# Kernel optimization log

Measured on AMD Instinct MI355X. Metric: run time of the kernel, lower is better.

The kernel has to match this reference:

```python
import jax, jax.numpy as jnp
import numpy as np

H, D = 16, 64  # n_heads, head_dim


def l2norm(t):
    # F.normalize(t, p=2, dim=-1)
    return t / jnp.maximum(jnp.linalg.norm(t, axis=-1, keepdims=True), 1e-12)


def setup_inputs() -> dict:
    key = jax.random.key(0)
    ks = jax.random.split(key, 6)
    B, N, C = 2, 2048, 1024
    x = jax.random.normal(ks[0], (B, N, C), jnp.float32)
    pos_bias = jax.random.normal(ks[1], (1, H, N, N), jnp.float32)
    mask = jnp.zeros((B, 1, 1, N), bool)  # attn_mask: True = masked
    Wqkv = jax.random.normal(ks[2], (C, 3 * H * D), jnp.float32) / np.sqrt(C)
    Wout = jax.random.normal(ks[3], (H * D, C), jnp.float32) / np.sqrt(H * D)
    Wpre = jax.random.normal(ks[4], (H, H), jnp.float32) / np.sqrt(H)   # 1x1 conv pre
    bpre = jnp.zeros((H,), jnp.float32)
    Wpost = jax.random.normal(ks[5], (H, H), jnp.float32) / np.sqrt(H)  # 1x1 conv post
    bpost = jnp.zeros((H,), jnp.float32)
    temperature = jnp.float32(15.5)
    return {"x": x, "pos_bias": pos_bias, "mask": mask, "Wqkv": Wqkv,
            "Wout": Wout, "Wpre": Wpre, "bpre": bpre, "Wpost": Wpost,
            "bpost": bpost, "temperature": temperature}


def reference(x, pos_bias, mask, Wqkv, Wout, Wpre, bpre, Wpost, bpost, temperature):
    B, N, C = x.shape
    # qkv: 'b n (h d qkv) -> qkv b h n d'
    qkv = (x @ Wqkv).reshape(B, N, H, D, 3)
    q = jnp.transpose(qkv[..., 0], (0, 2, 1, 3))  # [B,H,N,D]
    k = jnp.transpose(qkv[..., 1], (0, 2, 1, 3))
    v = jnp.transpose(qkv[..., 2], (0, 2, 1, 3))
    q, k = l2norm(q), l2norm(k)  # cosine_sim
    kv = jnp.stack([k, v], axis=0)  # attach_cache with cache=None
    # temperature-scaled cosine-sim scores
    dots = jnp.einsum('bhid,bhjd->bhij', q, k) * temperature
    # talking heads pre (1x1 conv over head channel)
    dots = jnp.einsum('gh,bhij->bgij', Wpre, dots) + bpre[None, :, None, None]
    dots = dots + pos_bias
    dots = jnp.where(mask, -jnp.finfo(dots.dtype).max, dots)
    attn = jax.nn.softmax(dots, axis=-1)
    # talking heads post
    attn = jnp.einsum('gh,bhij->bgij', Wpost, attn) + bpost[None, :, None, None]
    out = jnp.einsum('bhij,bhjd->bhid', attn, v)  # [B,H,N,D]
    out = jnp.transpose(out, (0, 2, 1, 3)).reshape(B, N, H * D) @ Wout
    return (out, kv)
```

## Files before the change

### kernel.cpp

```cpp
#include <hip/hip_runtime.h>
#include <stdint.h>

typedef __attribute__((ext_vector_type(8))) short bf16x8;
typedef __attribute__((ext_vector_type(4))) float f32x4;
typedef __attribute__((ext_vector_type(4))) short short4v;

#define DEV __device__ __forceinline__
#define L2E 1.4426950408889634f

DEV float bf2f(unsigned short s){ union{unsigned int u; float f;} x; x.u = ((unsigned int)s)<<16; return x.f; }
DEV unsigned short f2bf(float f){ union{float f; unsigned int u;} x; x.f = f; x.u += 0x7fffu + ((x.u>>16)&1u); return (unsigned short)(x.u>>16); }

DEV f32x4 mfma16(bf16x8 a, bf16x8 b, f32x4 c){
  return __builtin_amdgcn_mfma_f32_16x16x32_bf16(a, b, c, 0, 0, 0);
}
DEV f32x4 zero4(){ f32x4 z; z[0]=0.f; z[1]=0.f; z[2]=0.f; z[3]=0.f; return z; }
DEV bf16x8 zerob(){ bf16x8 z; z[0]=0;z[1]=0;z[2]=0;z[3]=0;z[4]=0;z[5]=0;z[6]=0;z[7]=0; return z; }
DEV float fexp2(float x){ float r; asm volatile("v_exp_f32 %0, %1" : "=v"(r) : "v"(x)); return r; }
DEV void barw(){ asm volatile("s_waitcnt lgkmcnt(0)" ::: "memory"); __builtin_amdgcn_s_barrier(); }

__global__ __launch_bounds__(256) void k_f32_to_bf16(const float* __restrict__ in, unsigned short* __restrict__ out, int n4){
  int i = blockIdx.x*256 + threadIdx.x;
  if (i < n4){
    float4 v = ((const float4*)in)[i];
    short4v o; o.x=(short)f2bf(v.x); o.y=(short)f2bf(v.y); o.z=(short)f2bf(v.z); o.w=(short)f2bf(v.w);
    ((short4v*)out)[i] = o;
  }
}

__global__ __launch_bounds__(256) void k_convT(const float* __restrict__ in, unsigned short* __restrict__ out, int R, int Cc){
  __shared__ float t[32][33];
  int c0 = blockIdx.x*32, r0 = blockIdx.y*32;
  int tid = threadIdx.x;
  int row = tid>>3, col4 = (tid&7)*4;
  float4 v = *(const float4*)&in[(size_t)(r0+row)*Cc + c0 + col4];
  t[row][col4+0]=v.x; t[row][col4+1]=v.y; t[row][col4+2]=v.z; t[row][col4+3]=v.w;
  __syncthreads();
  short4v o;
  o.x=(short)f2bf(t[col4+0][row]); o.y=(short)f2bf(t[col4+1][row]);
  o.z=(short)f2bf(t[col4+2][row]); o.w=(short)f2bf(t[col4+3][row]);
  *(short4v*)&out[(size_t)(c0+row)*R + r0 + col4] = o;
}

__global__ __launch_bounds__(256) void k_prep(const float* __restrict__ wpre, const float* __restrict__ wpost,
                                              const float* __restrict__ temp,
                                              unsigned short* __restrict__ wpre_t2,
                                              unsigned short* __restrict__ wpost_b){
  int t = threadIdx.x;
  float T = temp[0];
  wpre_t2[t] = f2bf(wpre[t]*T*L2E);
  wpost_b[t] = f2bf(wpost[t]);
}

__global__ __launch_bounds__(256) void k_maskf(const unsigned char* __restrict__ mask, float* __restrict__ maskf){
  int i = blockIdx.x*256 + threadIdx.x;
  if (i < 4096) maskf[i] = mask[i] ? -1e30f : 0.f;
}

template<int OUTF>
__global__ __launch_bounds__(256,2) void k_gemm(const unsigned short* __restrict__ A, const unsigned short* __restrict__ Bt,
                                                void* __restrict__ Cv, int M, int Nn, int K){
  __shared__ unsigned short As[128][72];
  __shared__ unsigned short Bs[128][72];
  int tid = threadIdx.x;
  int n0 = blockIdx.x*128, m0 = blockIdx.y*128;
  int w = tid>>6, lane = tid&63, lg = lane>>4, lp = lane&15;
  int wm = (w>>1)*64, wn = (w&1)*64;
  f32x4 acc[4][4];
  #pragma unroll
  for (int i=0;i<4;++i)
    #pragma unroll
    for (int j=0;j<4;++j) acc[i][j] = zero4();

  for (int kt=0; kt<K; kt+=64){
    #pragma unroll
    for (int cch=0; cch<4; ++cch){
      int e = tid + cch*256; int r = e>>3, cl = (e&7)*8;
      *(bf16x8*)&As[r][cl] = *(const bf16x8*)&A[(size_t)(m0+r)*K + kt + cl];
      *(bf16x8*)&Bs[r][cl] = *(const bf16x8*)&Bt[(size_t)(n0+r)*K + kt + cl];
    }
    __syncthreads();
    #pragma unroll
    for (int ks=0; ks<2; ++ks){
      bf16x8 a[4], b[4];
      #pragma unroll
      for (int mi=0; mi<4; ++mi) a[mi] = *(const bf16x8*)&As[wm+mi*16+lp][ks*32 + lg*8];
      #pragma unroll
      for (int ni=0; ni<4; ++ni) b[ni] = *(const bf16x8*)&Bs[wn+ni*16+lp][ks*32 + lg*8];
      #pragma unroll
      for (int mi=0; mi<4; ++mi)
        #pragma unroll
        for (int ni=0; ni<4; ++ni)
          acc[mi][ni] = mfma16(a[mi], b[ni], acc[mi][ni]);
    }
    __syncthreads();
  }
  #pragma unroll
  for (int mi=0; mi<4; ++mi)
    #pragma unroll
    for (int ni=0; ni<4; ++ni)
      #pragma unroll
      for (int r=0; r<4; ++r){
        int row = m0+wm+mi*16+lg*4+r, col = n0+wn+ni*16+lp;
        if (OUTF) ((float*)Cv)[(size_t)row*Nn+col] = acc[mi][ni][r];
        else ((unsigned short*)Cv)[(size_t)row*Nn+col] = f2bf(acc[mi][ni][r]);
      }
}

__global__ __launch_bounds__(256) void k_split_norm(const unsigned short* __restrict__ qkv,
                                                    unsigned short* __restrict__ q, unsigned short* __restrict__ k,
                                                    unsigned short* __restrict__ v, float* __restrict__ kv_out){
  int w = threadIdx.x>>6, lane = threadIdx.x&63;
  int widx = blockIdx.x*4 + w;
  int h = widx & 15; int bn = widx >> 4;
  int b = bn >> 11; int n = bn & 2047;
  size_t base = (size_t)bn*3072 + h*192 + lane*3;
  float qv = bf2f(qkv[base]), kvv = bf2f(qkv[base+1]), vv = bf2f(qkv[base+2]);
  float nq = qv*qv, nk = kvv*kvv;
  #pragma unroll
  for (int m=1; m<64; m<<=1){ nq += __shfl_xor(nq, m); nk += __shfl_xor(nk, m); }
  float qn = qv / fmaxf(sqrtf(nq), 1e-12f);
  float kn = kvv / fmaxf(sqrtf(nk), 1e-12f);
  size_t idx = ((size_t)(b*16+h)*2048 + n)*64 + lane;
  q[idx] = f2bf(qn); k[idx] = f2bf(kn); v[idx] = f2bf(vv);
  kv_out[idx] = kn;
  kv_out[4194304 + idx] = vv;
}

__global__ __launch_bounds__(256) void k_transpose_v(const unsigned short* __restrict__ v, unsigned short* __restrict__ vt){
  __shared__ unsigned short t[64][72];
  int bh = blockIdx.y; int n0 = blockIdx.x*64;
  int tid = threadIdx.x;
  #pragma unroll
  for (int cch=0; cch<2; ++cch){
    int e = tid + cch*256; int r = e>>3, c8 = (e&7)*8;
    *(bf16x8*)&t[r][c8] = *(const bf16x8*)&v[((size_t)bh*2048 + n0 + r)*64 + c8];
  }
  __syncthreads();
  #pragma unroll
  for (int cch=0; cch<2; ++cch){
    int e = tid + cch*256; int d = e>>3, nn8 = (e&7)*8;
    bf16x8 o;
    #pragma unroll
    for (int i=0;i<8;++i) o[i] = (short)t[nn8+i][d];
    *(bf16x8*)&vt[((size_t)bh*64 + d)*2048 + n0 + nn8] = o;
  }
}

__global__ __launch_bounds__(256) void k_vsum(const unsigned short* __restrict__ v, float* __restrict__ vsum){
  int bg = blockIdx.x;
  int d = threadIdx.x & 63, part = threadIdx.x>>6;
  float s = 0.f;
  for (int n = part*512; n < part*512+512; ++n) s += bf2f(v[((size_t)bg*2048 + n)*64 + d]);
  __shared__ float red[4][64];
  red[part][d] = s; __syncthreads();
  if (part==0) vsum[bg*64 + d] = red[0][d]+red[1][d]+red[2][d]+red[3][d];
}

__global__ __launch_bounds__(512,2) void k_score3(
    const unsigned short* __restrict__ q,
    const unsigned short* __restrict__ kk,
    const float* __restrict__ pos_bias,
    const float* __restrict__ maskf,
    const unsigned short* __restrict__ wpre_t2,
    const float* __restrict__ bpre,
    unsigned short* __restrict__ Pb,
    float* __restrict__ part_l)
{
  __shared__ __align__(16) char smem[40960];
  const int tid = threadIdx.x;
  const int w = tid>>6, lane = tid&63, lg = lane>>4, lp = lane&15;
  const int bid = blockIdx.x;
  const int qd = bid>>4, r2 = bid&15;
  const int b = r2>>3, n = qd*8 + (r2&7);
  const int it = n>>2, js = n&3;
  const int i0 = it*16, jsb = js*512;
  const int mbase = b*2048;

  bf16x8 qf[2][2];
  #pragma unroll
  for (int hh=0; hh<2; ++hh){
    const unsigned short* qb = q + ((size_t)(b*16+2*w+hh)*2048 + i0 + lp)*64;
    qf[hh][0] = *(const bf16x8*)(qb + lg*8);
    qf[hh][1] = *(const bf16x8*)(qb + 32 + lg*8);
  }
  bf16x8 preA = zerob();
  if (lg < 2) preA = *(const bf16x8*)&wpre_t2[lp*16 + lg*8];
  float bpre_s[4];
  #pragma unroll
  for (int r=0;r<4;++r) bpre_s[r] = bpre[lg*4+r]*L2E - 32.0f;

  float sacc[2][4];
  #pragma unroll
  for (int ii=0;ii<2;++ii)
    #pragma unroll
    for (int r=0;r<4;++r) sacc[ii][r] = 0.f;

  const size_t kbase0 = (size_t)(b*16 + 2*w)*131072;
  const size_t kbase1 = (size_t)(b*16 + 2*w+1)*131072;
  const size_t pb_lane = (size_t)(i0 + 2*w)*2048 + lp;

  bf16x8 k0v[4], k1v[4];
  #pragma unroll
  for (int kf=0; kf<2; ++kf)
    #pragma unroll
    for (int jf=0; jf<2; ++jf){
      size_t off = (size_t)(jsb + jf*16 + lp)*64 + kf*32 + lg*8;
      k0v[kf*2+jf] = *(const bf16x8*)(kk + kbase0 + off);
      k1v[kf*2+jf] = *(const bf16x8*)(kk + kbase1 + off);
    }
  float pbA[4][4], pbB[4][4];
  float mkA0, mkA1, mkB0, mkB1;
  #pragma unroll
  for (int cc=0; cc<4; ++cc)
    #pragma unroll
    for (int r=0;r<4;++r)
      pbA[cc][r] = pos_bias[(size_t)(lg*4+r)*4194304 + pb_lane + (size_t)(cc>>1)*2048 + (cc&1)*16 + jsb];
  mkA0 = maskf[mbase + jsb + lp];
  mkA1 = maskf[mbase + jsb + 16 + lp];

  for (int tt=0; tt<8; ++tt){
    {
      const int j0 = jsb + (2*tt)*32;
      const int j1 = jsb + (2*tt+1)*32;
      char* sbuf = smem;
      f32x4 s0[2], s1[2];
      #pragma unroll
      for (int jf=0;jf<2;++jf){ s0[jf]=zero4(); s1[jf]=zero4(); }
      #pragma unroll
      for (int kf=0; kf<2; ++kf)
        #pragma unroll
        for (int jf=0; jf<2; ++jf){
          s0[jf] = mfma16(qf[0][kf], k0v[kf*2+jf], s0[jf]);
          s1[jf] = mfma16(qf[1][kf], k1v[kf*2+jf], s1[jf]);
        }
      #pragma unroll
      for (int jf=0;jf<2;++jf)
        #pragma unroll
        for (int r=0;r<4;++r){
          int ij = (lg*4+r)*32 + jf*16 + lp;
          unsigned int pk = (unsigned int)f2bf(s0[jf][r]) | ((unsigned int)f2bf(s1[jf][r])<<16);
          *(unsigned int*)(sbuf + ij*40 + w*4) = pk;
        }
      #pragma unroll
      for (int kf=0; kf<2; ++kf)
        #pragma unroll
        for (int jf=0; jf<2; ++jf){
          size_t off = (size_t)(j1 + jf*16 + lp)*64 + kf*32 + lg*8;
          k0v[kf*2+jf] = *(const bf16x8*)(kk + kbase0 + off);
          k1v[kf*2+jf] = *(const bf16x8*)(kk + kbase1 + off);
        }
      #pragma unroll
      for (int cc=0; cc<4; ++cc)
        #pragma unroll
        for (int r=0;r<4;++r)
          pbB[cc][r] = pos_bias[(size_t)(lg*4+r)*4194304 + pb_lane + (size_t)(cc>>1)*2048 + (cc&1)*16 + j1];
      mkB0 = maskf[mbase + j1 + lp];
      mkB1 = maskf[mbase + j1 + 16 + lp];
      barw();
      #pragma unroll
      for (int cc=0; cc<4; ++cc){
        int c = w*4+cc;
        int il = 2*w + (cc>>1);
        int jl = (cc&1)*16 + lp;
        bf16x8 sfrag = zerob();
        if (lg < 2) sfrag = *(const bf16x8*)(sbuf + (c*16+lp)*40 + lg*16);
        f32x4 pa = mfma16(preA, sfrag, zero4());
        float mkj = (cc&1) ? mkA1 : mkA0;
        float pv0 = fexp2(fmaf(pbA[cc][0], L2E, pa[0] + bpre_s[0] + mkj));
        float pv1 = fexp2(fmaf(pbA[cc][1], L2E, pa[1] + bpre_s[1] + mkj));
        float pv2 = fexp2(fmaf(pbA[cc][2], L2E, pa[2] + bpre_s[2] + mkj));
        float pv3 = fexp2(fmaf(pbA[cc][3], L2E, pa[3] + bpre_s[3] + mkj));
        sacc[cc>>1][0] += pv0; sacc[cc>>1][1] += pv1;
        sacc[cc>>1][2] += pv2; sacc[cc>>1][3] += pv3;
        short4v p4;
        p4.x = (short)f2bf(pv0); p4.y = (short)f2bf(pv1);
        p4.z = (short)f2bf(pv2); p4.w = (short)f2bf(pv3);
        *(short4v*)&Pb[(((size_t)(b*2048 + i0+il)*2048) + j0 + jl)*16 + lg*4] = p4;
      }
    }
    {
      const int j0 = jsb + (2*tt+1)*32;
      const int j1 = jsb + ((2*tt+2)&15)*32;
      char* sbuf = smem + 20480;
      f32x4 s0[2], s1[2];
      #pragma unroll
      for (int jf=0;jf<2;++jf){ s0[jf]=zero4(); s1[jf]=zero4(); }
      #pragma unroll
      for (int kf=0; kf<2; ++kf)
        #pragma unroll
        for (int jf=0; jf<2; ++jf){
          s0[jf] = mfma16(qf[0][kf], k0v[kf*2+jf], s0[jf]);
          s1[jf] = mfma16(qf[1][kf], k1v[kf*2+jf], s1[jf]);
        }
      #pragma unroll
      for (int jf=0;jf<2;++jf)
        #pragma unroll
        for (int r=0;r<4;++r){
          int ij = (lg*4+r)*32 + jf*16 + lp;
          unsigned int pk = (unsigned int)f2bf(s0[jf][r]) | ((unsigned int)f2bf(s1[jf][r])<<16);
          *(unsigned int*)(sbuf + ij*40 + w*4) = pk;
        }
      #pragma unroll
      for (int kf=0; kf<2; ++kf)
        #pragma unroll
        for (int jf=0; jf<2; ++jf){
          size_t off = (size_t)(j1 + jf*16 + lp)*64 + kf*32 + lg*8;
          k0v[kf*2+jf] = *(const bf16x8*)(kk + kbase0 + off);
          k1v[kf*2+jf] = *(const bf16x8*)(kk + kbase1 + off);
        }
      #pragma unroll
      for (int cc=0; cc<4; ++cc)
        #pragma unroll
        for (int r=0;r<4;++r)
          pbA[cc][r] = pos_bias[(size_t)(lg*4+r)*4194304 + pb_lane + (size_t)(cc>>1)*2048 + (cc&1)*16 + j1];
      mkA0 = maskf[mbase + j1 + lp];
      mkA1 = maskf[mbase + j1 + 16 + lp];
      barw();
      #pragma unroll
      for (int cc=0; cc<4; ++cc){
        int c = w*4+cc;
        int il = 2*w + (cc>>1);
        int jl = (cc&1)*16 + lp;
        bf16x8 sfrag = zerob();
        if (lg < 2) sfrag = *(const bf16x8*)(sbuf + (c*16+lp)*40 + lg*16);
        f32x4 pa = mfma16(preA, sfrag, zero4());
        float mkj = (cc&1) ? mkB1 : mkB0;
        float pv0 = fexp2(fmaf(pbB[cc][0], L2E, pa[0] + bpre_s[0] + mkj));
        float pv1 = fexp2(fmaf(pbB[cc][1], L2E, pa[1] + bpre_s[1] + mkj));
        float pv2 = fexp2(fmaf(pbB[cc][2], L2E, pa[2] + bpre_s[2] + mkj));
        float pv3 = fexp2(fmaf(pbB[cc][3], L2E, pa[3] + bpre_s[3] + mkj));
        sacc[cc>>1][0] += pv0; sacc[cc>>1][1] += pv1;
        sacc[cc>>1][2] += pv2; sacc[cc>>1][3] += pv3;
        short4v p4;
        p4.x = (short)f2bf(pv0); p4.y = (short)f2bf(pv1);
        p4.z = (short)f2bf(pv2); p4.w = (short)f2bf(pv3);
        *(short4v*)&Pb[(((size_t)(b*2048 + i0+il)*2048) + j0 + jl)*16 + lg*4] = p4;
      }
    }
  }

  #pragma unroll
  for (int ii=0;ii<2;++ii)
    #pragma unroll
    for (int r=0;r<4;++r){
      float v = sacc[ii][r];
      #pragma unroll
      for (int m=1; m<16; m<<=1) v += __shfl_xor(v, m);
      sacc[ii][r] = v;
    }
  if (lp == 0){
    int base = ((b*128+it)*4 + js)*256;
    #pragma unroll
    for (int ii=0;ii<2;++ii){
      float4 st; st.x = sacc[ii][0]; st.y = sacc[ii][1]; st.z = sacc[ii][2]; st.w = sacc[ii][3];
      *(float4*)&part_l[base + (2*w+ii)*16 + lg*4] = st;
    }
  }
}

__global__ __launch_bounds__(512,2) void k_mix3(
    const unsigned short* __restrict__ Pb,
    const unsigned short* __restrict__ vt,
    const unsigned short* __restrict__ wpost_b,
    const float* __restrict__ bpost,
    const float* __restrict__ vsum,
    const float* __restrict__ part_l,
    float* __restrict__ pout0,
    float* __restrict__ pout1)
{
  __shared__ __align__(16) char smem[33792];
  float* linv = (float*)(smem + 32768);
  const int tid = threadIdx.x;
  const int w = tid>>6, lane = tid&63, lg = lane>>4, lp = lane&15;
  const int bid = blockIdx.x;
  const int qd = bid>>4, r2 = bid&15;
  const int b = r2>>3, n = qd*8 + (r2&7);
  const int it = n>>1, js = n&1;
  const int i0 = it*16, jsb = js*1024;

  if (tid < 256){
    int base = ((b*128+it)*4)*256 + tid;
    float sum = part_l[base] + part_l[base+256] + part_l[base+512] + part_l[base+768];
    linv[tid] = 1.f/sum;
  }
  __syncthreads();

  bf16x8 postB[2];
  #pragma unroll
  for (int ii=0;ii<2;++ii){
    postB[ii] = zerob();
    if (lg < 2){
      bf16x8 wf = *(const bf16x8*)&wpost_b[lp*16 + lg*8];
      int i = 2*w+ii;
      #pragma unroll
      for (int e=0;e<8;++e){
        float vsc = bf2f((unsigned short)wf[e]) * linv[i*16 + lg*8 + e];
        postB[ii][e] = (short)f2bf(vsc);
      }
    }
  }

  f32x4 oacc[2][4];
  #pragma unroll
  for (int hh=0; hh<2; ++hh)
    #pragma unroll
    for (int df=0; df<4; ++df) oacc[hh][df] = zero4();

  bf16x8 pA[4], pB[4];
  #pragma unroll
  for (int cc=0; cc<4; ++cc){
    int il = 2*w + (cc>>1);
    pA[cc] = zerob();
    if (lg < 2)
      pA[cc] = *(const bf16x8*)&Pb[(((size_t)(b*2048 + i0+il)*2048) + jsb + (cc&1)*16 + lp)*16 + lg*8];
  }
  __syncthreads();

  for (int tt=0; tt<16; ++tt){
    {
      const int j0 = jsb + (2*tt)*32;
      const int j1 = jsb + (2*tt+1)*32;
      char* abuf = smem;
      #pragma unroll
      for (int cc=0; cc<4; ++cc){
        int il = 2*w + (cc>>1);
        pB[cc] = zerob();
        if (lg < 2)
          pB[cc] = *(const bf16x8*)&Pb[(((size_t)(b*2048 + i0+il)*2048) + j1 + (cc&1)*16 + lp)*16 + lg*8];
      }
      bf16x8 vfr[2][4];
      #pragma unroll
      for (int hh=0; hh<2; ++hh)
        #pragma unroll
        for (int df=0; df<4; ++df)
          vfr[hh][df] = *(const bf16x8*)(vt + ((size_t)(b*16+2*w+hh)*64 + df*16 + lp)*2048 + j0 + lg*8);
      #pragma unroll
      for (int cc=0; cc<4; ++cc){
        int il = 2*w + (cc>>1);
        f32x4 aa = mfma16(pA[cc], postB[cc>>1], zero4());
        short4v av;
        av.x = (short)f2bf(aa[0]); av.y = (short)f2bf(aa[1]);
        av.z = (short)f2bf(aa[2]); av.w = (short)f2bf(aa[3]);
        int row = lp*16 + il;
        int chunk = ((cc&1)*4 + lg) ^ ((lp ^ il)&6);
        *(short4v*)(abuf + row*64 + chunk*8) = av;
      }
      barw();
      #pragma unroll
      for (int hh=0; hh<2; ++hh){
        int gg = 2*w+hh;
        bf16x8 af = *(const bf16x8*)(abuf + (gg*16+lp)*64 + (((lg*2) ^ ((gg^lp)&6))*8));
        #pragma unroll
        for (int df=0; df<4; ++df)
          oacc[hh][df] = mfma16(af, vfr[hh][df], oacc[hh][df]);
      }
    }
    {
      const int j0 = jsb + (2*tt+1)*32;
      const int j1 = jsb + ((2*tt+2)&31)*32;
      char* abuf = smem + 16384;
      #pragma unroll
      for (int cc=0; cc<4; ++cc){
        int il = 2*w + (cc>>1);
        pA[cc] = zerob();
        if (lg < 2)
          pA[cc] = *(const bf16x8*)&Pb[(((size_t)(b*2048 + i0+il)*2048) + j1 + (cc&1)*16 + lp)*16 + lg*8];
      }
      bf16x8 vfr[2][4];
      #pragma unroll
      for (int hh=0; hh<2; ++hh)
        #pragma unroll
        for (int df=0; df<4; ++df)
          vfr[hh][df] = *(const bf16x8*)(vt + ((size_t)(b*16+2*w+hh)*64 + df*16 + lp)*2048 + j0 + lg*8);
      #pragma unroll
      for (int cc=0; cc<4; ++cc){
        int il = 2*w + (cc>>1);
        f32x4 aa = mfma16(pB[cc], postB[cc>>1], zero4());
        short4v av;
        av.x = (short)f2bf(aa[0]); av.y = (short)f2bf(aa[1]);
        av.z = (short)f2bf(aa[2]); av.w = (short)f2bf(aa[3]);
        int row = lp*16 + il;
        int chunk = ((cc&1)*4 + lg) ^ ((lp ^ il)&6);
        *(short4v*)(abuf + row*64 + chunk*8) = av;
      }
      barw();
      #pragma unroll
      for (int hh=0; hh<2; ++hh){
        int gg = 2*w+hh;
        bf16x8 af = *(const bf16x8*)(abuf + (gg*16+lp)*64 + (((lg*2) ^ ((gg^lp)&6))*8));
        #pragma unroll
        for (int df=0; df<4; ++df)
          oacc[hh][df] = mfma16(af, vfr[hh][df], oacc[hh][df]);
      }
    }
  }

  float* po = js ? pout1 : pout0;
  #pragma unroll
  for (int hh=0; hh<2; ++hh){
    int gg = 2*w+hh;
    float bp = (js==0) ? bpost[gg] : 0.f;
    #pragma unroll
    for (int df=0; df<4; ++df){
      int d = df*16+lp;
      float vs = vsum[(b*16+gg)*64 + d];
      #pragma unroll
      for (int r=0;r<4;++r){
        po[((size_t)b*2048 + i0 + lg*4 + r)*1024 + gg*64 + d] = oacc[hh][df][r] + bp*vs;
      }
    }
  }
}

__global__ __launch_bounds__(256) void k_combine(const float* __restrict__ p0, const float* __restrict__ p1,
                                                 unsigned short* __restrict__ ao){
  int i = blockIdx.x*256 + threadIdx.x;
  float4 a = ((const float4*)p0)[i];
  float4 c = ((const float4*)p1)[i];
  short4v o;
  o.x=(short)f2bf(a.x+c.x); o.y=(short)f2bf(a.y+c.y);
  o.z=(short)f2bf(a.z+c.z); o.w=(short)f2bf(a.w+c.w);
  ((short4v*)ao)[i] = o;
}

extern "C" void kernel_launch(void* const* d_in, const int* in_sizes, int n_in,
                              void* d_out, int out_size, void* d_ws, size_t ws_size,
                              hipStream_t stream)
{
  const float* x        = (const float*)d_in[0];
  const float* pos_bias = (const float*)d_in[1];
  const unsigned char* mask = (const unsigned char*)d_in[2];
  const float* Wqkv     = (const float*)d_in[3];
  const float* Wout     = (const float*)d_in[4];
  const float* Wpre     = (const float*)d_in[5];
  const float* bpre     = (const float*)d_in[6];
  const float* Wpost    = (const float*)d_in[7];
  const float* bpost    = (const float*)d_in[8];
  const float* temp     = (const float*)d_in[9];
  float* out = (float*)d_out;
  float* kv_out = out + 4194304;

  char* ws = (char*)d_ws;
  unsigned short* XB    = (unsigned short*)(ws + 0);
  unsigned short* WT    = (unsigned short*)(ws + 8388608);
  unsigned short* WOT   = (unsigned short*)(ws + 8388608);
  float*          PART_L= (float*)        (ws + 11534336);
  unsigned short* WPRE2 = (unsigned short*)(ws + 12583424);
  unsigned short* WPOST = (unsigned short*)(ws + 12583936);
  float*          VSUM  = (float*)        (ws + 12584448);
  float*          MASKF = (float*)        (ws + 12593152);
  unsigned short* QKV   = (unsigned short*)(ws + 14680064);
  unsigned short* VT    = (unsigned short*)(ws + 14680064);
  float*          POUT0 = (float*)        (ws + 23068672);
  unsigned short* Q     = (unsigned short*)(ws + 39845888);
  unsigned short* KB    = (unsigned short*)(ws + 48234496);
  unsigned short* VB    = (unsigned short*)(ws + 56623104);
  float*          POUT1 = (float*)        (ws + 56623104);
  unsigned short* PB    = (unsigned short*)(ws + 75497472);
  unsigned short* AO    = XB;

  k_f32_to_bf16<<<4096, 256, 0, stream>>>(x, XB, 1048576);
  k_convT<<<dim3(96,32), 256, 0, stream>>>(Wqkv, WT, 1024, 3072);
  k_gemm<0><<<dim3(24,32), 256, 0, stream>>>(XB, WT, (void*)QKV, 4096, 3072, 1024);
  k_split_norm<<<16384, 256, 0, stream>>>(QKV, Q, KB, VB, kv_out);
  k_transpose_v<<<dim3(32,32), 256, 0, stream>>>(VB, VT);
  k_vsum<<<32, 256, 0, stream>>>(VB, VSUM);
  k_prep<<<1, 256, 0, stream>>>(Wpre, Wpost, temp, WPRE2, WPOST);
  k_maskf<<<16, 256, 0, stream>>>(mask, MASKF);
  k_convT<<<dim3(32,32), 256, 0, stream>>>(Wout, WOT, 1024, 1024);

  k_score3<<<1024, 512, 0, stream>>>(Q, KB, pos_bias, MASKF, WPRE2, bpre, PB, PART_L);
  k_mix3<<<512, 512, 0, stream>>>(PB, VT, WPOST, bpost, VSUM, PART_L, POUT0, POUT1);
  k_combine<<<4096, 256, 0, stream>>>(POUT0, POUT1, AO);
  k_gemm<1><<<dim3(8,32), 256, 0, stream>>>(AO, WOT, d_out, 4096, 1024, 1024);
}
```

Measured before the change: 549.6 us.

## Precompute exp(pos_bias) as head-interleaved fp16 and simplify mix loop

Adds a pre-pass that computes exp(pos_bias) once, stores it in fp16 with the 16 heads interleaved per (i,j), and has the score kernel multiply by it instead of reading strided fp32 pos_bias per head. This halves pos_bias bytes in the score kernel and gives contiguous per-lane loads. The cost is an extra full read of the 268MB fp32 pos_bias plus a 134MB write in a separate kernel, along with fp16 range and precision risk for exp of large biases. The mix kernel loses its software prefetch of P fragments in favour of a simpler single loop, and its launch bound is raised to request 4 blocks per unit.

```diff
diff --git a/kernel.cpp b/kernel.cpp
--- a/kernel.cpp
+++ b/kernel.cpp
@@ -1,4 +1,5 @@
 #include <hip/hip_runtime.h>
+#include <hip/hip_fp16.h>
 #include <stdint.h>
 
 typedef __attribute__((ext_vector_type(8))) short bf16x8;
@@ -10,6 +11,8 @@
 
 DEV float bf2f(unsigned short s){ union{unsigned int u; float f;} x; x.u = ((unsigned int)s)<<16; return x.f; }
 DEV unsigned short f2bf(float f){ union{float f; unsigned int u;} x; x.f = f; x.u += 0x7fffu + ((x.u>>16)&1u); return (unsigned short)(x.u>>16); }
+DEV float h2f(unsigned short u){ return __half2float(__ushort_as_half(u)); }
+DEV unsigned short f2h(float f){ return __half_as_ushort(__float2half(f)); }
 
 DEV f32x4 mfma16(bf16x8 a, bf16x8 b, f32x4 c){
   return __builtin_amdgcn_mfma_f32_16x16x32_bf16(a, b, c, 0, 0, 0);
@@ -57,6 +60,23 @@
   if (i < 4096) maskf[i] = mask[i] ? -1e30f : 0.f;
 }
 
+__global__ __launch_bounds__(256) void k_pbexp(const float* __restrict__ pb, unsigned short* __restrict__ epb){
+  int idx = blockIdx.x*256 + threadIdx.x;
+  int i = idx >> 11, j = idx & 2047;
+  unsigned int pk[8];
+  #pragma unroll
+  for (int g2=0; g2<8; ++g2){
+    float a = fexp2(pb[(size_t)(2*g2  )*4194304 + (size_t)i*2048 + j] * L2E);
+    float b = fexp2(pb[(size_t)(2*g2+1)*4194304 + (size_t)i*2048 + j] * L2E);
+    pk[g2] = (unsigned int)f2h(a) | ((unsigned int)f2h(b)<<16);
+  }
+  uint4 o0, o1;
+  o0.x=pk[0]; o0.y=pk[1]; o0.z=pk[2]; o0.w=pk[3];
+  o1.x=pk[4]; o1.y=pk[5]; o1.z=pk[6]; o1.w=pk[7];
+  *(uint4*)&epb[(size_t)idx*16]     = o0;
+  *(uint4*)&epb[(size_t)idx*16 + 8] = o1;
+}
+
 template<int OUTF>
 __global__ __launch_bounds__(256,2) void k_gemm(const unsigned short* __restrict__ A, const unsigned short* __restrict__ Bt,
                                                 void* __restrict__ Cv, int M, int Nn, int K){
@@ -157,10 +177,10 @@
   if (part==0) vsum[bg*64 + d] = red[0][d]+red[1][d]+red[2][d]+red[3][d];
 }
 
-__global__ __launch_bounds__(512,2) void k_score3(
+__global__ __launch_bounds__(512,2) void k_score2(
     const unsigned short* __restrict__ q,
     const unsigned short* __restrict__ kk,
-    const float* __restrict__ pos_bias,
+    const unsigned short* __restrict__ epb,
     const float* __restrict__ maskf,
     const unsigned short* __restrict__ wpre_t2,
     const float* __restrict__ bpre,
@@ -198,7 +218,6 @@
 
   const size_t kbase0 = (size_t)(b*16 + 2*w)*131072;
   const size_t kbase1 = (size_t)(b*16 + 2*w+1)*131072;
-  const size_t pb_lane = (size_t)(i0 + 2*w)*2048 + lp;
 
   bf16x8 k0v[4], k1v[4];
   #pragma unroll
@@ -209,13 +228,13 @@
       k0v[kf*2+jf] = *(const bf16x8*)(kk + kbase0 + off);
       k1v[kf*2+jf] = *(const bf16x8*)(kk + kbase1 + off);
     }
-  float pbA[4][4], pbB[4][4];
+  short4v epA[4], epB[4];
   float mkA0, mkA1, mkB0, mkB1;
   #pragma unroll
-  for (int cc=0; cc<4; ++cc)
-    #pragma unroll
-    for (int r=0;r<4;++r)
-      pbA[cc][r] = pos_bias[(size_t)(lg*4+r)*4194304 + pb_lane + (size_t)(cc>>1)*2048 + (cc&1)*16 + jsb];
+  for (int cc=0; cc<4; ++cc){
+    int il = 2*w + (cc>>1);
+    epA[cc] = *(const short4v*)&epb[(((size_t)(i0+il)*2048) + jsb + (cc&1)*16 + lp)*16 + lg*4];
+  }
   mkA0 = maskf[mbase + jsb + lp];
   mkA1 = maskf[mbase + jsb + 16 + lp];
 
@@ -251,10 +270,10 @@
           k1v[kf*2+jf] = *(const bf16x8*)(kk + kbase1 + off);
         }
       #pragma unroll
-      for (int cc=0; cc<4; ++cc)
-        #pragma unroll
-        for (int r=0;r<4;++r)
-          pbB[cc][r] = pos_bias[(size_t)(lg*4+r)*4194304 + pb_lane + (size_t)(cc>>1)*2048 + (cc&1)*16 + j1];
+      for (int cc=0; cc<4; ++cc){
+        int il = 2*w + (cc>>1);
+        epB[cc] = *(const short4v*)&epb[(((size_t)(i0+il)*2048) + j1 + (cc&1)*16 + lp)*16 + lg*4];
+      }
       mkB0 = maskf[mbase + j1 + lp];
       mkB1 = maskf[mbase + j1 + 16 + lp];
       barw();
@@ -267,10 +286,10 @@
         if (lg < 2) sfrag = *(const bf16x8*)(sbuf + (c*16+lp)*40 + lg*16);
         f32x4 pa = mfma16(preA, sfrag, zero4());
         float mkj = (cc&1) ? mkA1 : mkA0;
-        float pv0 = fexp2(fmaf(pbA[cc][0], L2E, pa[0] + bpre_s[0] + mkj));
-        float pv1 = fexp2(fmaf(pbA[cc][1], L2E, pa[1] + bpre_s[1] + mkj));
-        float pv2 = fexp2(fmaf(pbA[cc][2], L2E, pa[2] + bpre_s[2] + mkj));
-        float pv3 = fexp2(fmaf(pbA[cc][3], L2E, pa[3] + bpre_s[3] + mkj));
+        float pv0 = fexp2(pa[0] + bpre_s[0] + mkj) * h2f((unsigned short)epA[cc][0]);
+        float pv1 = fexp2(pa[1] + bpre_s[1] + mkj) * h2f((unsigned short)epA[cc][1]);
+        float pv2 = fexp2(pa[2] + bpre_s[2] + mkj) * h2f((unsigned short)epA[cc][2]);
+        float pv3 = fexp2(pa[3] + bpre_s[3] + mkj) * h2f((unsigned short)epA[cc][3]);
         sacc[cc>>1][0] += pv0; sacc[cc>>1][1] += pv1;
         sacc[cc>>1][2] += pv2; sacc[cc>>1][3] += pv3;
         short4v p4;
@@ -310,10 +329,10 @@
           k1v[kf*2+jf] = *(const bf16x8*)(kk + kbase1 + off);
         }
       #pragma unroll
-      for (int cc=0; cc<4; ++cc)
-        #pragma unroll
-        for (int r=0;r<4;++r)
-          pbA[cc][r] = pos_bias[(size_t)(lg*4+r)*4194304 + pb_lane + (size_t)(cc>>1)*2048 + (cc&1)*16 + j1];
+      for (int cc=0; cc<4; ++cc){
+        int il = 2*w + (cc>>1);
+        epA[cc] = *(const short4v*)&epb[(((size_t)(i0+il)*2048) + j1 + (cc&1)*16 + lp)*16 + lg*4];
+      }
       mkA0 = maskf[mbase + j1 + lp];
       mkA1 = maskf[mbase + j1 + 16 + lp];
       barw();
@@ -326,10 +345,10 @@
         if (lg < 2) sfrag = *(const bf16x8*)(sbuf + (c*16+lp)*40 + lg*16);
         f32x4 pa = mfma16(preA, sfrag, zero4());
         float mkj = (cc&1) ? mkB1 : mkB0;
-        float pv0 = fexp2(fmaf(pbB[cc][0], L2E, pa[0] + bpre_s[0] + mkj));
-        float pv1 = fexp2(fmaf(pbB[cc][1], L2E, pa[1] + bpre_s[1] + mkj));
-        float pv2 = fexp2(fmaf(pbB[cc][2], L2E, pa[2] + bpre_s[2] + mkj));
-        float pv3 = fexp2(fmaf(pbB[cc][3], L2E, pa[3] + bpre_s[3] + mkj));
+        float pv0 = fexp2(pa[0] + bpre_s[0] + mkj) * h2f((unsigned short)epB[cc][0]);
+        float pv1 = fexp2(pa[1] + bpre_s[1] + mkj) * h2f((unsigned short)epB[cc][1]);
+        float pv2 = fexp2(pa[2] + bpre_s[2] + mkj) * h2f((unsigned short)epB[cc][2]);
+        float pv3 = fexp2(pa[3] + bpre_s[3] + mkj) * h2f((unsigned short)epB[cc][3]);
         sacc[cc>>1][0] += pv0; sacc[cc>>1][1] += pv1;
         sacc[cc>>1][2] += pv2; sacc[cc>>1][3] += pv3;
         short4v p4;
@@ -359,7 +378,7 @@
   }
 }
 
-__global__ __launch_bounds__(512,2) void k_mix3(
+__global__ __launch_bounds__(512,4) void k_mix(
     const unsigned short* __restrict__ Pb,
     const unsigned short* __restrict__ vt,
     const unsigned short* __restrict__ wpost_b,
@@ -407,92 +426,44 @@
     #pragma unroll
     for (int df=0; df<4; ++df) oacc[hh][df] = zero4();
 
-  bf16x8 pA[4], pB[4];
-  #pragma unroll
-  for (int cc=0; cc<4; ++cc){
-    int il = 2*w + (cc>>1);
-    pA[cc] = zerob();
-    if (lg < 2)
-      pA[cc] = *(const bf16x8*)&Pb[(((size_t)(b*2048 + i0+il)*2048) + jsb + (cc&1)*16 + lp)*16 + lg*8];
-  }
   __syncthreads();
 
-  for (int tt=0; tt<16; ++tt){
-    {
-      const int j0 = jsb + (2*tt)*32;
-      const int j1 = jsb + (2*tt+1)*32;
-      char* abuf = smem;
-      #pragma unroll
-      for (int cc=0; cc<4; ++cc){
-        int il = 2*w + (cc>>1);
-        pB[cc] = zerob();
-        if (lg < 2)
-          pB[cc] = *(const bf16x8*)&Pb[(((size_t)(b*2048 + i0+il)*2048) + j1 + (cc&1)*16 + lp)*16 + lg*8];
-      }
-      bf16x8 vfr[2][4];
-      #pragma unroll
-      for (int hh=0; hh<2; ++hh)
-        #pragma unroll
-        for (int df=0; df<4; ++df)
-          vfr[hh][df] = *(const bf16x8*)(vt + ((size_t)(b*16+2*w+hh)*64 + df*16 + lp)*2048 + j0 + lg*8);
-      #pragma unroll
-      for (int cc=0; cc<4; ++cc){
-        int il = 2*w + (cc>>1);
-        f32x4 aa = mfma16(pA[cc], postB[cc>>1], zero4());
-        short4v av;
-        av.x = (short)f2bf(aa[0]); av.y = (short)f2bf(aa[1]);
-        av.z = (short)f2bf(aa[2]); av.w = (short)f2bf(aa[3]);
-        int row = lp*16 + il;
-        int chunk = ((cc&1)*4 + lg) ^ ((lp ^ il)&6);
-        *(short4v*)(abuf + row*64 + chunk*8) = av;
-      }
-      barw();
-      #pragma unroll
-      for (int hh=0; hh<2; ++hh){
-        int gg = 2*w+hh;
-        bf16x8 af = *(const bf16x8*)(abuf + (gg*16+lp)*64 + (((lg*2) ^ ((gg^lp)&6))*8));
-        #pragma unroll
-        for (int df=0; df<4; ++df)
-          oacc[hh][df] = mfma16(af, vfr[hh][df], oacc[hh][df]);
-      }
-    }
-    {
-      const int j0 = jsb + (2*tt+1)*32;
-      const int j1 = jsb + ((2*tt+2)&31)*32;
-      char* abuf = smem + 16384;
-      #pragma unroll
-      for (int cc=0; cc<4; ++cc){
-        int il = 2*w + (cc>>1);
-        pA[cc] = zerob();
-        if (lg < 2)
-          pA[cc] = *(const bf16x8*)&Pb[(((size_t)(b*2048 + i0+il)*2048) + j1 + (cc&1)*16 + lp)*16 + lg*8];
-      }
-      bf16x8 vfr[2][4];
-      #pragma unroll
-      for (int hh=0; hh<2; ++hh)
-        #pragma unroll
-        for (int df=0; df<4; ++df)
-          vfr[hh][df] = *(const bf16x8*)(vt + ((size_t)(b*16+2*w+hh)*64 + df*16 + lp)*2048 + j0 + lg*8);
-      #pragma unroll
-      for (int cc=0; cc<4; ++cc){
-        int il = 2*w + (cc>>1);
-        f32x4 aa = mfma16(pB[cc], postB[cc>>1], zero4());
-        short4v av;
-        av.x = (short)f2bf(aa[0]); av.y = (short)f2bf(aa[1]);
-        av.z = (short)f2bf(aa[2]); av.w = (short)f2bf(aa[3]);
-        int row = lp*16 + il;
-        int chunk = ((cc&1)*4 + lg) ^ ((lp ^ il)&6);
-        *(short4v*)(abuf + row*64 + chunk*8) = av;
-      }
-      barw();
-      #pragma unroll
-      for (int hh=0; hh<2; ++hh){
-        int gg = 2*w+hh;
-        bf16x8 af = *(const bf16x8*)(abuf + (gg*16+lp)*64 + (((lg*2) ^ ((gg^lp)&6))*8));
-        #pragma unroll
-        for (int df=0; df<4; ++df)
-          oacc[hh][df] = mfma16(af, vfr[hh][df], oacc[hh][df]);
-      }
+  for (int t=0; t<32; ++t){
+    const int j0 = jsb + t*32;
+    char* abuf = smem + (t&1)*16384;
+    bf16x8 pfr[4];
+    #pragma unroll
+    for (int cc=0; cc<4; ++cc){
+      int il = 2*w + (cc>>1);
+      pfr[cc] = zerob();
+      if (lg < 2)
+        pfr[cc] = *(const bf16x8*)&Pb[(((size_t)(b*2048 + i0+il)*2048) + j0 + (cc&1)*16 + lp)*16 + lg*8];
+    }
+    bf16x8 vfr[2][4];
+    #pragma unroll
+    for (int hh=0; hh<2; ++hh)
+      #pragma unroll
+      for (int df=0; df<4; ++df)
+        vfr[hh][df] = *(const bf16x8*)(vt + ((size_t)(b*16+2*w+hh)*64 + df*16 + lp)*2048 + j0 + lg*8);
+    #pragma unroll
+    for (int cc=0; cc<4; ++cc){
+      int il = 2*w + (cc>>1);
+      f32x4 aa = mfma16(pfr[cc], postB[cc>>1], zero4());
+      short4v av;
+      av.x = (short)f2bf(aa[0]); av.y = (short)f2bf(aa[1]);
+      av.z = (short)f2bf(aa[2]); av.w = (short)f2bf(aa[3]);
+      int row = lp*16 + il;
+      int chunk = ((cc&1)*4 + lg) ^ ((lp ^ il)&6);
+      *(short4v*)(abuf + row*64 + chunk*8) = av;
+    }
+    barw();
+    #pragma unroll
+    for (int hh=0; hh<2; ++hh){
+      int gg = 2*w+hh;
+      bf16x8 af = *(const bf16x8*)(abuf + (gg*16+lp)*64 + (((lg*2) ^ ((gg^lp)&6))*8));
+      #pragma unroll
+      for (int df=0; df<4; ++df)
+        oacc[hh][df] = mfma16(af, vfr[hh][df], oacc[hh][df]);
     }
   }
 
@@ -558,6 +529,7 @@
   unsigned short* VB    = (unsigned short*)(ws + 56623104);
   float*          POUT1 = (float*)        (ws + 56623104);
   unsigned short* PB    = (unsigned short*)(ws + 75497472);
+  unsigned short* EPB   = (unsigned short*)(ws + 343932928);
   unsigned short* AO    = XB;
 
   k_f32_to_bf16<<<4096, 256, 0, stream>>>(x, XB, 1048576);
@@ -570,8 +542,9 @@
   k_maskf<<<16, 256, 0, stream>>>(mask, MASKF);
   k_convT<<<dim3(32,32), 256, 0, stream>>>(Wout, WOT, 1024, 1024);
 
-  k_score3<<<1024, 512, 0, stream>>>(Q, KB, pos_bias, MASKF, WPRE2, bpre, PB, PART_L);
-  k_mix3<<<512, 512, 0, stream>>>(PB, VT, WPOST, bpost, VSUM, PART_L, POUT0, POUT1);
+  k_pbexp<<<16384, 256, 0, stream>>>(pos_bias, EPB);
+  k_score2<<<1024, 512, 0, stream>>>(Q, KB, EPB, MASKF, WPRE2, bpre, PB, PART_L);
+  k_mix<<<512, 512, 0, stream>>>(PB, VT, WPOST, bpost, VSUM, PART_L, POUT0, POUT1);
   k_combine<<<4096, 256, 0, stream>>>(POUT0, POUT1, AO);
   k_gemm<1><<<dim3(8,32), 256, 0, stream>>>(AO, WOT, d_out, 4096, 1024, 1024);
 }
```

After: 596.1 us. 8.5% more time.
